# Performance work log

Hardware: AMD Instinct MI355X
Metric: run time of the kernel (lower is better)

The kernel has to match this reference:

```python
import jax, jax.numpy as jnp
import numpy as np

COMMITMENT_COST = 0.25


def setup_inputs() -> dict:
    key = jax.random.key(0)
    k1, k2 = jax.random.split(key)
    B, C, H, W = 64, 256, 32, 32
    K, D = 4096, 256
    x = jax.random.normal(k1, (B, C, H, W), dtype=jnp.float32)
    # original init: uniform(-1/K, 1/K)
    embedding = jax.random.uniform(k2, (K, D), dtype=jnp.float32,
                                   minval=-1.0 / K, maxval=1.0 / K)
    return {"x": x, "embedding": embedding}


def reference(x, embedding):
    # x: [B, C, H, W] with C == embedding_dim; embedding: [K, D]
    K, D = embedding.shape
    xt = jnp.transpose(x, (0, 2, 3, 1))            # [B, H, W, D]
    flat = xt.reshape(-1, D)                        # [N, D]
    N = flat.shape[0]

    distances = (jnp.sum(flat * flat, axis=1, keepdims=True)
                 + jnp.sum(embedding * embedding, axis=1)
                 - 2.0 * flat @ embedding.T)
    idx = jnp.argmin(distances, axis=1)             # [N] int32

    # one-hot @ embedding == gather
    quantized = embedding[idx].reshape(xt.shape)    # [B, H, W, D]

    e_latent_loss = jnp.mean((jax.lax.stop_gradient(quantized) - xt) ** 2)
    q_latent_loss = jnp.mean((quantized - jax.lax.stop_gradient(xt)) ** 2)
    loss = q_latent_loss + COMMITMENT_COST * e_latent_loss

    # straight-through estimator
    quantized_st = xt + jax.lax.stop_gradient(quantized - xt)

    # perplexity from code usage histogram
    counts = jnp.zeros((K,), dtype=jnp.float32).at[idx].add(1.0)
    avg_probs = counts / jnp.float32(N)
    perplexity = jnp.exp(-jnp.sum(avg_probs * jnp.log(avg_probs + 1e-10)))

    out = jnp.transpose(quantized_st, (0, 3, 1, 2))  # back to [B, C, H, W]
    return out, loss, perplexity
```

## Files before the change

### kernel.cpp

```cpp
#include <hip/hip_runtime.h>
#include <hip/hip_bf16.h>


#define K_CODES 4096

typedef __attribute__((ext_vector_type(8))) short bf16x8;
typedef __attribute__((ext_vector_type(4))) float f32x4;
typedef __attribute__((ext_vector_type(8))) unsigned short u16x8;

__device__ __forceinline__ void gload_lds16(const void* g, void* l) {
    __builtin_amdgcn_global_load_lds((const __attribute__((address_space(1))) unsigned int*)g,
                                     (__attribute__((address_space(3))) unsigned int*)l,
                                     16, 0, 0);
}

__device__ __forceinline__ unsigned short f2bf(float v) {
    __hip_bfloat16 h = __float2bfloat16(v);
    return *(unsigned short*)&h;
}

__global__ __launch_bounds__(64) void vq_prep_emb(const float* __restrict__ emb,
                                                  unsigned short* __restrict__ embB,
                                                  float* __restrict__ Se) {
    const int k = blockIdx.x, t = threadIdx.x;
    const float* e = emb + ((size_t)k << 8) + t * 4;
    float4 v = *(const float4*)e;
    ushort4 o;
    o.x = f2bf(v.x); o.y = f2bf(v.y); o.z = f2bf(v.z); o.w = f2bf(v.w);
    *(ushort4*)(embB + ((size_t)k << 8) + t * 4) = o;
    float s = v.x * v.x + v.y * v.y + v.z * v.z + v.w * v.w;
#pragma unroll
    for (int m = 1; m < 64; m <<= 1) s += __shfl_xor(s, m, 64);
    if (t == 0) Se[k] = s;
}

__global__ __launch_bounds__(256) void vq_transpose(const float* __restrict__ x,
                                                    unsigned short* __restrict__ xT) {
    __shared__ float tile[64][65];
    const int bid = blockIdx.x;
    const int ht = bid & 15, ct = (bid >> 4) & 3, b = bid >> 6;
    const int hw0 = ht * 64, c0 = ct * 64;
    const int t = threadIdx.x;
    {
        const int hwl = t & 63, cl = t >> 6;
        const float* xp = x + ((size_t)b << 18) + ((size_t)c0 << 10) + hw0 + hwl;
#pragma unroll
        for (int i = 0; i < 16; ++i)
            tile[cl + i * 4][hwl] = xp[(size_t)(cl + i * 4) << 10];
    }
    __syncthreads();
    {
        const int hwl = t >> 2, cs = (t & 3) * 16;
        unsigned short* op = xT + ((size_t)(b * 1024 + hw0 + hwl) << 8) + c0 + cs;
        u16x8 p0, p1;
#pragma unroll
        for (int j = 0; j < 8; ++j) p0[j] = f2bf(tile[cs + j][hwl]);
#pragma unroll
        for (int j = 0; j < 8; ++j) p1[j] = f2bf(tile[cs + 8 + j][hwl]);
        *(u16x8*)op = p0;
        *(u16x8*)(op + 8) = p1;
    }
}

__global__ __launch_bounds__(128, 1) void vq_argmin_mfma(
    const unsigned short* __restrict__ xT,
    const unsigned short* __restrict__ embB,
    const float* __restrict__ Se,
    int* __restrict__ idx_out,
    unsigned int* __restrict__ counts) {
    extern __shared__ char smem[];
    char* xsb = smem;
    char* esb = smem + 65536;

    const int t = threadIdx.x;
    const int w = t >> 6;
    const int l = t & 63;
    const int g = l >> 4;
    const int r = l & 15;
    const int n0 = blockIdx.x * 128;
    const int wrow = w * 64;
    const int swz = (r & 7) << 4;

#pragma unroll
    for (int i = 0; i < 32; ++i) {
        const int obase = (w * 32 + i) * 1024;
        const int o = obase + l * 16;
        const int row = o >> 9;
        const int scol = (o & 511) ^ ((row & 7) << 4);
        gload_lds16(xT + ((size_t)(n0 + row) << 8) + (scol >> 1), xsb + obase);
    }

    float best[16];
    int bidx[16];
#pragma unroll
    for (int i = 0; i < 16; ++i) { best[i] = 1e30f; bidx[i] = 0; }

    for (int cb = 0; cb < K_CODES; cb += 128) {
        f32x4 acc[4][8];
#pragma unroll
        for (int rf = 0; rf < 4; ++rf)
#pragma unroll
            for (int f = 0; f < 8; ++f) acc[rf][f] = (f32x4){0.f, 0.f, 0.f, 0.f};

        for (int dk = 0; dk < 256; dk += 64) {
            __syncthreads();
#pragma unroll
            for (int i = 0; i < 8; ++i) {
                const int obase = (w * 8 + i) * 1024;
                const int o = obase + l * 16;
                const int row = o >> 7;
                const int scol = (o & 127) ^ ((row & 7) << 4);
                gload_lds16(embB + ((size_t)(cb + row) << 8) + dk + (scol >> 1),
                            esb + obase);
            }
            __syncthreads();

#pragma unroll
            for (int ks = 0; ks < 2; ++ks) {
                const int colA = (dk + ks * 32 + g * 8) * 2;
                const int colB = (ks * 32 + g * 8) * 2;
                const int cA = colA ^ swz;
                const int cB = colB ^ swz;
                bf16x8 af[4];
#pragma unroll
                for (int rf = 0; rf < 4; ++rf) {
                    const int row = wrow + rf * 16 + r;
                    af[rf] = *(const bf16x8*)(xsb + row * 512 + cA);
                }
#pragma unroll
                for (int f = 0; f < 8; ++f) {
                    const int row = f * 16 + r;
                    bf16x8 bv = *(const bf16x8*)(esb + row * 128 + cB);
#pragma unroll
                    for (int rf = 0; rf < 4; ++rf)
                        acc[rf][f] = __builtin_amdgcn_mfma_f32_16x16x32_bf16(
                            af[rf], bv, acc[rf][f], 0, 0, 0);
                }
            }
        }

#pragma unroll
        for (int f = 0; f < 8; ++f) {
            const float se = Se[cb + f * 16 + r];
            const int c = cb + f * 16 + r;
#pragma unroll
            for (int rf = 0; rf < 4; ++rf)
#pragma unroll
                for (int reg = 0; reg < 4; ++reg) {
                    const float s = fmaf(-2.0f, acc[rf][f][reg], se);
                    const int sl = rf * 4 + reg;
                    if (s < best[sl]) { best[sl] = s; bidx[sl] = c; }
                }
        }
    }

#pragma unroll
    for (int sl = 0; sl < 16; ++sl) {
        float bs = best[sl];
        int bi = bidx[sl];
#pragma unroll
        for (int m = 1; m < 16; m <<= 1) {
            const float os = __shfl_xor(bs, m, 64);
            const int oi = __shfl_xor(bi, m, 64);
            if (os < bs || (os == bs && oi < bi)) { bs = os; bi = oi; }
        }
        if (r == 0) {
            const int rf = sl >> 2, reg = sl & 3;
            const int row = n0 + wrow + rf * 16 + g * 4 + reg;
            idx_out[row] = bi;
            atomicAdd(&counts[bi], 1u);
        }
    }
}

__global__ __launch_bounds__(256) void vq_out(const float* __restrict__ x,
                                              const float* __restrict__ emb,
                                              const int* __restrict__ idx,
                                              float* __restrict__ out,
                                              double* __restrict__ loss_acc) {
    __shared__ double sd[256];
    const int t = threadIdx.x;
    const int bc = blockIdx.x;
    const int b = bc >> 8, c = bc & 255;
    const size_t base = (size_t)bc << 10;
    const int hw = t * 4;
    float4 xv = *(const float4*)(x + base + hw);
    int4 iv = *(const int4*)(idx + (b << 10) + hw);
    const float q0 = emb[((size_t)iv.x << 8) + c];
    const float q1 = emb[((size_t)iv.y << 8) + c];
    const float q2 = emb[((size_t)iv.z << 8) + c];
    const float q3 = emb[((size_t)iv.w << 8) + c];
    const float d0 = q0 - xv.x, d1 = q1 - xv.y, d2 = q2 - xv.z, d3 = q3 - xv.w;
    float4 o;
    o.x = xv.x + d0;
    o.y = xv.y + d1;
    o.z = xv.z + d2;
    o.w = xv.w + d3;
    *(float4*)(out + base + hw) = o;
    sd[t] = (double)d0 * d0 + (double)d1 * d1 + (double)d2 * d2 + (double)d3 * d3;
    __syncthreads();
    for (int off = 128; off > 0; off >>= 1) {
        if (t < off) sd[t] += sd[t + off];
        __syncthreads();
    }
    if (t == 0) atomicAdd(loss_acc, sd[0]);
}

__global__ __launch_bounds__(256) void vq_final(const unsigned int* __restrict__ counts,
                                                const double* __restrict__ loss_acc,
                                                float* __restrict__ out_scalars) {
    __shared__ double sd[256];
    const int t = threadIdx.x;
    double s = 0.0;
    for (int j = t; j < K_CODES; j += 256) {
        const double p = (double)counts[j] * (1.0 / 65536.0);
        s += p * log(p + 1e-10);
    }
    sd[t] = s;
    __syncthreads();
    for (int off = 128; off > 0; off >>= 1) {
        if (t < off) sd[t] += sd[t + off];
        __syncthreads();
    }
    if (t == 0) {
        const double mse = loss_acc[0] / 16777216.0;
        out_scalars[0] = (float)(1.25 * mse);
        out_scalars[1] = (float)exp(-sd[0]);
    }
}

extern "C" void kernel_launch(void* const* d_in, const int* in_sizes, int n_in,
                              void* d_out, int out_size, void* d_ws, size_t ws_size,
                              hipStream_t stream) {
    const float* x = (const float*)d_in[0];
    const float* emb = (const float*)d_in[1];
    float* out = (float*)d_out;

    char* ws = (char*)d_ws;
    double* loss_acc = (double*)ws;
    unsigned int* counts = (unsigned int*)(ws + 1024);
    float* Se = (float*)(ws + 20480);
    int* idx = (int*)(ws + 36864);
    unsigned short* embB = (unsigned short*)(ws + 299008);
    unsigned short* xT = (unsigned short*)(ws + 2396160);

    hipMemsetAsync(ws, 0, 20480, stream);
    vq_prep_emb<<<K_CODES, 64, 0, stream>>>(emb, embB, Se);
    vq_transpose<<<4096, 256, 0, stream>>>(x, xT);
    vq_argmin_mfma<<<512, 128, 81920, stream>>>(xT, embB, Se, idx, counts);
    vq_out<<<64 * 256, 256, 0, stream>>>(x, emb, idx, out, loss_acc);
    vq_final<<<1, 256, 0, stream>>>(counts, loss_acc, out + (out_size - 2));
}
```

Before: 600.3 us.

## Pack distance and code index into max-key, split codebook across waves

Measured after the change: 770.5 us. +28.4%, slower.

```diff
diff --git a/kernel.cpp b/kernel.cpp
--- a/kernel.cpp
+++ b/kernel.cpp
@@ -21,7 +21,7 @@
 
 __global__ __launch_bounds__(64) void vq_prep_emb(const float* __restrict__ emb,
                                                   unsigned short* __restrict__ embB,
-                                                  float* __restrict__ Se) {
+                                                  float* __restrict__ SeN) {
     const int k = blockIdx.x, t = threadIdx.x;
     const float* e = emb + ((size_t)k << 8) + t * 4;
     float4 v = *(const float4*)e;
@@ -31,7 +31,7 @@
     float s = v.x * v.x + v.y * v.y + v.z * v.z + v.w * v.w;
 #pragma unroll
     for (int m = 1; m < 64; m <<= 1) s += __shfl_xor(s, m, 64);
-    if (t == 0) Se[k] = s;
+    if (t == 0) SeN[k] = -0.5f * s;
 }
 
 __global__ __launch_bounds__(256) void vq_transpose(const float* __restrict__ x,
@@ -62,122 +62,108 @@
     }
 }
 
-__global__ __launch_bounds__(128, 1) void vq_argmin_mfma(
+__global__ __launch_bounds__(256, 2) void vq_argmin_mfma(
     const unsigned short* __restrict__ xT,
     const unsigned short* __restrict__ embB,
-    const float* __restrict__ Se,
-    int* __restrict__ idx_out,
-    unsigned int* __restrict__ counts) {
-    extern __shared__ char smem[];
-    char* xsb = smem;
-    char* esb = smem + 65536;
+    const float* __restrict__ SeN,
+    unsigned int* __restrict__ keys) {
+    extern __shared__ char xsb[];
 
     const int t = threadIdx.x;
     const int w = t >> 6;
     const int l = t & 63;
-    const int g = l >> 4;
+    const int h = l >> 4;
     const int r = l & 15;
     const int n0 = blockIdx.x * 128;
-    const int wrow = w * 64;
-    const int swz = (r & 7) << 4;
-
-#pragma unroll
-    for (int i = 0; i < 32; ++i) {
-        const int obase = (w * 32 + i) * 1024;
+
+#pragma unroll
+    for (int i = 0; i < 16; ++i) {
+        const int obase = (w * 16 + i) * 1024;
         const int o = obase + l * 16;
         const int row = o >> 9;
-        const int scol = (o & 511) ^ ((row & 7) << 4);
+        const int scol = (o & 511) ^ ((row & 15) << 4);
         gload_lds16(xT + ((size_t)(n0 + row) << 8) + (scol >> 1), xsb + obase);
     }
-
-    float best[16];
-    int bidx[16];
-#pragma unroll
-    for (int i = 0; i < 16; ++i) { best[i] = 1e30f; bidx[i] = 0; }
-
-    for (int cb = 0; cb < K_CODES; cb += 128) {
-        f32x4 acc[4][8];
-#pragma unroll
-        for (int rf = 0; rf < 4; ++rf)
-#pragma unroll
-            for (int f = 0; f < 8; ++f) acc[rf][f] = (f32x4){0.f, 0.f, 0.f, 0.f};
-
-        for (int dk = 0; dk < 256; dk += 64) {
-            __syncthreads();
-#pragma unroll
-            for (int i = 0; i < 8; ++i) {
-                const int obase = (w * 8 + i) * 1024;
-                const int o = obase + l * 16;
-                const int row = o >> 7;
-                const int scol = (o & 127) ^ ((row & 7) << 4);
-                gload_lds16(embB + ((size_t)(cb + row) << 8) + dk + (scol >> 1),
-                            esb + obase);
+    __syncthreads();
+
+    unsigned int best[32];
+#pragma unroll
+    for (int s = 0; s < 32; ++s) best[s] = 0u;
+
+    const int swz = r << 4;
+
+    for (int ch = 0; ch < 16; ++ch) {
+        const int cb = w * 1024 + ch * 64;
+        float nh[4];
+        unsigned int lowb[4];
+#pragma unroll
+        for (int cf = 0; cf < 4; ++cf) {
+            nh[cf] = SeN[cb + cf * 16 + r];
+            lowb[cf] = 4095u - (unsigned int)(cb + cf * 16 + r);
+        }
+        f32x4 acc[8][4];
+#pragma unroll
+        for (int rf = 0; rf < 8; ++rf)
+#pragma unroll
+            for (int cf = 0; cf < 4; ++cf)
+                acc[rf][cf] = (f32x4){nh[cf], nh[cf], nh[cf], nh[cf]};
+
+        const unsigned short* pB0 = embB + ((size_t)(cb + r) << 8) + h * 8;
+
+#pragma unroll
+        for (int dkk = 0; dkk < 8; ++dkk) {
+            const int dk = dkk * 32;
+            bf16x8 bv[4];
+#pragma unroll
+            for (int cf = 0; cf < 4; ++cf)
+                bv[cf] = *(const bf16x8*)(pB0 + cf * 4096 + dk);
+            bf16x8 af[8];
+#pragma unroll
+            for (int rf = 0; rf < 8; ++rf) {
+                const int row = rf * 16 + r;
+                af[rf] = *(const bf16x8*)(xsb + row * 512 + (((dk + h * 8) * 2) ^ swz));
             }
-            __syncthreads();
-
-#pragma unroll
-            for (int ks = 0; ks < 2; ++ks) {
-                const int colA = (dk + ks * 32 + g * 8) * 2;
-                const int colB = (ks * 32 + g * 8) * 2;
-                const int cA = colA ^ swz;
-                const int cB = colB ^ swz;
-                bf16x8 af[4];
-#pragma unroll
-                for (int rf = 0; rf < 4; ++rf) {
-                    const int row = wrow + rf * 16 + r;
-                    af[rf] = *(const bf16x8*)(xsb + row * 512 + cA);
+#pragma unroll
+            for (int cf = 0; cf < 4; ++cf)
+#pragma unroll
+                for (int rf = 0; rf < 8; ++rf)
+                    acc[rf][cf] = __builtin_amdgcn_mfma_f32_16x16x32_bf16(
+                        af[rf], bv[cf], acc[rf][cf], 0, 0, 0);
+        }
+
+#pragma unroll
+        for (int rf = 0; rf < 8; ++rf)
+#pragma unroll
+            for (int cf = 0; cf < 4; ++cf)
+#pragma unroll
+                for (int reg = 0; reg < 4; ++reg) {
+                    const unsigned int u = __float_as_uint(acc[rf][cf][reg]);
+                    unsigned int key = u ^ (0x80000000u | (unsigned int)((int)u >> 31));
+                    key = (key & 0xFFFFF000u) | lowb[cf];
+                    const int s = rf * 4 + reg;
+                    best[s] = best[s] > key ? best[s] : key;
                 }
-#pragma unroll
-                for (int f = 0; f < 8; ++f) {
-                    const int row = f * 16 + r;
-                    bf16x8 bv = *(const bf16x8*)(esb + row * 128 + cB);
-#pragma unroll
-                    for (int rf = 0; rf < 4; ++rf)
-                        acc[rf][f] = __builtin_amdgcn_mfma_f32_16x16x32_bf16(
-                            af[rf], bv, acc[rf][f], 0, 0, 0);
-                }
-            }
+    }
+
+#pragma unroll
+    for (int s = 0; s < 32; ++s) {
+        unsigned int k = best[s];
+#pragma unroll
+        for (int m = 1; m <= 8; m <<= 1) {
+            const unsigned int o = __shfl_xor(k, m, 64);
+            k = k > o ? k : o;
         }
-
-#pragma unroll
-        for (int f = 0; f < 8; ++f) {
-            const float se = Se[cb + f * 16 + r];
-            const int c = cb + f * 16 + r;
-#pragma unroll
-            for (int rf = 0; rf < 4; ++rf)
-#pragma unroll
-                for (int reg = 0; reg < 4; ++reg) {
-                    const float s = fmaf(-2.0f, acc[rf][f][reg], se);
-                    const int sl = rf * 4 + reg;
-                    if (s < best[sl]) { best[sl] = s; bidx[sl] = c; }
-                }
-        }
-    }
-
-#pragma unroll
-    for (int sl = 0; sl < 16; ++sl) {
-        float bs = best[sl];
-        int bi = bidx[sl];
-#pragma unroll
-        for (int m = 1; m < 16; m <<= 1) {
-            const float os = __shfl_xor(bs, m, 64);
-            const int oi = __shfl_xor(bi, m, 64);
-            if (os < bs || (os == bs && oi < bi)) { bs = os; bi = oi; }
-        }
-        if (r == 0) {
-            const int rf = sl >> 2, reg = sl & 3;
-            const int row = n0 + wrow + rf * 16 + g * 4 + reg;
-            idx_out[row] = bi;
-            atomicAdd(&counts[bi], 1u);
-        }
+        if (r == 0)
+            atomicMax(&keys[n0 + (s >> 2) * 16 + h * 4 + (s & 3)], k);
     }
 }
 
 __global__ __launch_bounds__(256) void vq_out(const float* __restrict__ x,
                                               const float* __restrict__ emb,
-                                              const int* __restrict__ idx,
+                                              const unsigned int* __restrict__ keys,
                                               float* __restrict__ out,
-                                              double* __restrict__ loss_acc) {
+                                              double* __restrict__ loss_acc,
+                                              unsigned int* __restrict__ counts) {
     __shared__ double sd[256];
     const int t = threadIdx.x;
     const int bc = blockIdx.x;
@@ -185,11 +171,21 @@
     const size_t base = (size_t)bc << 10;
     const int hw = t * 4;
     float4 xv = *(const float4*)(x + base + hw);
-    int4 iv = *(const int4*)(idx + (b << 10) + hw);
-    const float q0 = emb[((size_t)iv.x << 8) + c];
-    const float q1 = emb[((size_t)iv.y << 8) + c];
-    const float q2 = emb[((size_t)iv.z << 8) + c];
-    const float q3 = emb[((size_t)iv.w << 8) + c];
+    uint4 kv = *(const uint4*)(keys + (b << 10) + hw);
+    const int c0 = 4095 - (int)(kv.x & 0xFFFu);
+    const int c1 = 4095 - (int)(kv.y & 0xFFFu);
+    const int c2 = 4095 - (int)(kv.z & 0xFFFu);
+    const int c3 = 4095 - (int)(kv.w & 0xFFFu);
+    if (c == 0) {
+        atomicAdd(&counts[c0], 1u);
+        atomicAdd(&counts[c1], 1u);
+        atomicAdd(&counts[c2], 1u);
+        atomicAdd(&counts[c3], 1u);
+    }
+    const float q0 = emb[((size_t)c0 << 8) + c];
+    const float q1 = emb[((size_t)c1 << 8) + c];
+    const float q2 = emb[((size_t)c2 << 8) + c];
+    const float q3 = emb[((size_t)c3 << 8) + c];
     const float d0 = q0 - xv.x, d1 = q1 - xv.y, d2 = q2 - xv.z, d3 = q3 - xv.w;
     float4 o;
     o.x = xv.x + d0;
@@ -239,15 +235,15 @@
     char* ws = (char*)d_ws;
     double* loss_acc = (double*)ws;
     unsigned int* counts = (unsigned int*)(ws + 1024);
-    float* Se = (float*)(ws + 20480);
-    int* idx = (int*)(ws + 36864);
-    unsigned short* embB = (unsigned short*)(ws + 299008);
-    unsigned short* xT = (unsigned short*)(ws + 2396160);
-
-    hipMemsetAsync(ws, 0, 20480, stream);
-    vq_prep_emb<<<K_CODES, 64, 0, stream>>>(emb, embB, Se);
+    unsigned int* keys = (unsigned int*)(ws + 17408);
+    float* SeN = (float*)(ws + 279552);
+    unsigned short* embB = (unsigned short*)(ws + 295936);
+    unsigned short* xT = (unsigned short*)(ws + 2393088);
+
+    hipMemsetAsync(ws, 0, 279552, stream);
+    vq_prep_emb<<<K_CODES, 64, 0, stream>>>(emb, embB, SeN);
     vq_transpose<<<4096, 256, 0, stream>>>(x, xT);
-    vq_argmin_mfma<<<512, 128, 81920, stream>>>(xT, embB, Se, idx, counts);
-    vq_out<<<64 * 256, 256, 0, stream>>>(x, emb, idx, out, loss_acc);
+    vq_argmin_mfma<<<512, 256, 65536, stream>>>(xT, embB, SeN, keys);
+    vq_out<<<64 * 256, 256, 0, stream>>>(x, emb, keys, out, loss_acc, counts);
     vq_final<<<1, 256, 0, stream>>>(counts, loss_acc, out + (out_size - 2));
 }
```
